# Optimization experiments

Measured on AMD Instinct MI355X. Metric: run time of the kernel, lower is better.

## Reference

```python
import jax, jax.numpy as jnp
import numpy as np

DIM = 256
H = 4
K = 16
R = 4
EPS = 1e-5


def _conv1x1(x, W, b):
    # x: [B, Cin, N, P], W: [Cout, Cin], b: [Cout]
    return jnp.einsum('oc,bcnp->bonp', W, x) + b[None, :, None, None]


def setup_inputs() -> dict:
    key = jax.random.key(0)
    ks = jax.random.split(key, 12)
    B, N = 4, 8192
    s = 1.0 / np.sqrt(DIM)
    inp = {
        'queries': jax.random.normal(ks[0], (B, DIM, N, R), dtype=jnp.float32),
        'feats': jax.random.normal(ks[1], (B, DIM, N, K), dtype=jnp.float32),
        'Wq': jax.random.normal(ks[2], (DIM, DIM), dtype=jnp.float32) * s,
        'bq': jnp.zeros((DIM,), dtype=jnp.float32),
        'Wk': jax.random.normal(ks[3], (DIM, DIM), dtype=jnp.float32) * s,
        'bk': jnp.zeros((DIM,), dtype=jnp.float32),
        'Wv': jax.random.normal(ks[4], (DIM, DIM), dtype=jnp.float32) * s,
        'bv': jnp.zeros((DIM,), dtype=jnp.float32),
        'W1': jax.random.normal(ks[5], (2 * DIM, DIM), dtype=jnp.float32) * s,
        'b1': jnp.zeros((2 * DIM,), dtype=jnp.float32),
        'gamma': jnp.ones((2 * DIM,), dtype=jnp.float32),
        'beta': jnp.zeros((2 * DIM,), dtype=jnp.float32),
        'W2': jax.random.normal(ks[6], (DIM, 2 * DIM), dtype=jnp.float32) * (1.0 / np.sqrt(2 * DIM)),
        'b2': jnp.zeros((DIM,), dtype=jnp.float32),
    }
    return inp


def reference(queries, feats, Wq, bq, Wk, bk, Wv, bv, W1, b1, gamma, beta, W2, b2):
    B, _, N, _ = feats.shape
    d = DIM // H
    queries_iden = queries  # [B, dim, N, r]

    q = _conv1x1(queries, Wq, bq).reshape(B, H, d, N, R)   # [B,h,d,N,r]
    k = _conv1x1(feats, Wk, bk).reshape(B, H, d, N, K)     # [B,h,d,N,K]
    v = _conv1x1(feats, Wv, bv).reshape(B, H, d, N, K)     # [B,h,d,N,K]

    # logits: [B,N,h,r,K]
    logits = jnp.einsum('bhdnr,bhdnk->bnhrk', q, k) * (d ** -0.5)
    soft = jax.nn.softmax(logits, axis=-1)
    # agg: [B,N,h,r,d] -> permute to [B,N,h,d,r] -> [B,N,dim,r] -> [B,dim,N,r]
    agg = jnp.einsum('bnhrk,bhdnk->bnhdr', soft, v)
    agg = agg.reshape(B, N, DIM, R).transpose(0, 2, 1, 3)
    agg = agg + queries_iden

    # FFN: conv1x1 -> BN (training-mode batch stats) -> ReLU -> conv1x1, residual, ReLU
    h1 = _conv1x1(agg, W1, b1)  # [B, 2*dim, N, r]
    mean = jnp.mean(h1, axis=(0, 2, 3), keepdims=True)
    var = jnp.var(h1, axis=(0, 2, 3), keepdims=True)
    h1 = (h1 - mean) * jax.lax.rsqrt(var + EPS)
    h1 = h1 * gamma[None, :, None, None] + beta[None, :, None, None]
    h1 = jax.nn.relu(h1)
    h2 = _conv1x1(h1, W2, b2)
    return jax.nn.relu(h2 + agg)
```

## Files before the change

kernel.cpp:

```cpp
#include <hip/hip_runtime.h>
#include <hip/hip_bf16.h>

#define NB 4
#define NRQ 32768
#define NKF 131072

using u16 = unsigned short;
typedef short bf16x8 __attribute__((ext_vector_type(8)));
typedef float f32x4  __attribute__((ext_vector_type(4)));
typedef u16   u16x8  __attribute__((ext_vector_type(8)));
typedef u16   u16x4  __attribute__((ext_vector_type(4)));
typedef u16   u16x2  __attribute__((ext_vector_type(2)));

#if defined(__has_builtin)
#  if __has_builtin(__builtin_amdgcn_fdot2_f32_bf16)
#    define HAVE_DOT2 1
#  endif
#endif
#ifndef HAVE_DOT2
#  define HAVE_DOT2 0
#endif

#if HAVE_DOT2
typedef __bf16 bfv2 __attribute__((ext_vector_type(2)));
union bpack { bf16x8 v; bfv2 p[4]; };
__device__ __forceinline__ float dot2(bfv2 a, bfv2 b, float c){
  return __builtin_amdgcn_fdot2_f32_bf16(a, b, c, false);
}
#endif
union vpack { bf16x8 v; u16 e[8]; };

__device__ __forceinline__ u16 f2b(float f){
  unsigned u = __float_as_uint(f);
  return (u16)((u + 0x7fffu + ((u >> 16) & 1u)) >> 16);
}
__device__ __forceinline__ float b2f(u16 v){
  return __uint_as_float(((unsigned)v) << 16);
}

#define GLOAD16(g, l) __builtin_amdgcn_global_load_lds( \
    (const __attribute__((address_space(1))) unsigned int*)(g), \
    (__attribute__((address_space(3))) unsigned int*)(l), 16, 0, 0)

__global__ __launch_bounds__(256) void cvtW_k(
    const float* __restrict__ Wk, const float* __restrict__ Wv,
    const float* __restrict__ Wq, const float* __restrict__ W1,
    const float* __restrict__ W2, u16* __restrict__ wT)
{
  long e = ((long)blockIdx.x * 256 + threadIdx.x) * 8;
  const float* src; long off;
  if      (e < 65536)  { src = Wk; off = e; }
  else if (e < 131072) { src = Wv; off = e - 65536; }
  else if (e < 196608) { src = Wq; off = e - 131072; }
  else if (e < 327680) { src = W1; off = e - 196608; }
  else                 { src = W2; off = e - 327680; }
  float4 f0 = *reinterpret_cast<const float4*>(src + off);
  float4 f1 = *reinterpret_cast<const float4*>(src + off + 4);
  u16x8 p;
  p[0]=f2b(f0.x); p[1]=f2b(f0.y); p[2]=f2b(f0.z); p[3]=f2b(f0.w);
  p[4]=f2b(f1.x); p[5]=f2b(f1.y); p[6]=f2b(f1.z); p[7]=f2b(f1.w);
  *reinterpret_cast<u16x8*>(wT + e) = p;
}

__global__ void prep_k(const float* __restrict__ bk, const float* __restrict__ bv,
                       float* __restrict__ bKV, float* __restrict__ stats)
{
  int i = blockIdx.x * 256 + threadIdx.x;
  if (i < 512)       bKV[i] = (i < 256) ? bk[i] : bv[i - 256];
  else               stats[i - 512] = 0.f;
}

__global__ __launch_bounds__(256) void transpose_k(
    const float* __restrict__ in, u16* __restrict__ out,
    int NCtot, long outBatch)
{
  __shared__ u16 sT[64][264];
  const int t = threadIdx.x, b = blockIdx.y;
  const int nr0 = blockIdx.x * 64;
  const int cb = t >> 2, nrq = t & 3;
  const long ib = (long)b * 256 * NCtot + nr0;

  #pragma unroll
  for (int ci = 0; ci < 4; ++ci){
    const int c = cb + ci * 64;
    const float* src = in + ib + (long)c * NCtot + nrq * 16;
    #pragma unroll
    for (int j = 0; j < 4; ++j){
      float4 f = *reinterpret_cast<const float4*>(src + j * 4);
      int nr = nrq * 16 + j * 4;
      sT[nr+0][c] = f2b(f.x); sT[nr+1][c] = f2b(f.y);
      sT[nr+2][c] = f2b(f.z); sT[nr+3][c] = f2b(f.w);
    }
  }
  __syncthreads();
  const int row = t >> 2, qtr = t & 3;
  u16* orow = out + (long)b * outBatch + (long)(nr0 + row) * 256 + qtr * 64;
  #pragma unroll
  for (int i = 0; i < 8; ++i)
    *reinterpret_cast<u16x8*>(orow + i * 8) =
        *reinterpret_cast<const u16x8*>(&sT[row][qtr * 64 + i * 8]);
}

template<int MODE, int KD>
__global__ __launch_bounds__(256) void gemm_k(
    const u16* __restrict__ A, long aBatch, int chTiles,
    const u16* __restrict__ Wb, const float* __restrict__ bias,
    u16* __restrict__ outH, long oBatch, int NCH,
    float* __restrict__ statSum, float* __restrict__ statSq,
    const u16* __restrict__ residT,
    float* __restrict__ outF, long fBatch)
{
  __shared__ __align__(16) char sA[2][16384];
  __shared__ __align__(16) char sB[2][16384];

  const int t = threadIdx.x, lane = t & 63, wid = t >> 6;
  const int wm = wid >> 1, wn = wid & 1;
  const int b = blockIdx.z;

  const int nwg = gridDim.x, orig = blockIdx.x;
  const int qq = nwg >> 3, rr = nwg & 7, xcd = orig & 7, pos = orig >> 3;
  const int wg = (xcd < rr ? xcd * (qq + 1) : rr * (qq + 1) + (xcd - rr) * qq) + pos;
  const int rowT = wg / chTiles, chT = wg % chTiles;

  const u16* Ab = A + (long)b * aBatch + (long)rowT * 128 * KD;
  const u16* Wt = Wb + (long)chT * 128 * KD;
  const int sub = lane >> 3, kc8 = ((lane & 7) ^ sub) * 8;

  f32x4 acc[4][4];
  #pragma unroll
  for (int i = 0; i < 4; ++i)
    #pragma unroll
    for (int j = 0; j < 4; ++j) acc[i][j] = (f32x4){0.f,0.f,0.f,0.f};

  auto STAGE = [&](int buf, int ks){
    const int k0 = ks * 64;
    #pragma unroll
    for (int i = 0; i < 4; ++i){
      const int chunk = wid * 4 + i;
      GLOAD16(Ab + (long)(chunk*8 + sub)*KD + k0 + kc8, sA[buf] + chunk*1024);
      GLOAD16(Wt + (long)(chunk*8 + sub)*KD + k0 + kc8, sB[buf] + chunk*1024);
    }
  };

  constexpr int NT = KD / 64;
  STAGE(0, 0);
  __syncthreads();
  int cur = 0;
  for (int ks = 0; ks < NT; ++ks){
    if (ks + 1 < NT) STAGE(cur ^ 1, ks + 1);
    const char* pA = sA[cur]; const char* pB = sB[cur];
    #pragma unroll
    for (int kk = 0; kk < 2; ++kk){
      bf16x8 af[4], bf[4];
      #pragma unroll
      for (int mi = 0; mi < 4; ++mi){
        int m = wm*64 + mi*16 + (lane & 15);
        af[mi] = *reinterpret_cast<const bf16x8*>(
            pA + ((m*128 + kk*64 + (lane>>4)*16) ^ ((m & 7) << 4)));
      }
      #pragma unroll
      for (int ni = 0; ni < 4; ++ni){
        int c = wn*64 + ni*16 + (lane & 15);
        bf[ni] = *reinterpret_cast<const bf16x8*>(
            pB + ((c*128 + kk*64 + (lane>>4)*16) ^ ((c & 7) << 4)));
      }
      #pragma unroll
      for (int mi = 0; mi < 4; ++mi)
        #pragma unroll
        for (int ni = 0; ni < 4; ++ni)
          acc[mi][ni] = __builtin_amdgcn_mfma_f32_16x16x32_bf16(
              af[mi], bf[ni], acc[mi][ni], 0, 0, 0);
    }
    __syncthreads();
    cur ^= 1;
  }

  int chI[4]; float bv[4];
  #pragma unroll
  for (int ni = 0; ni < 4; ++ni){
    int ch = chT*128 + wn*64 + ni*16 + (lane & 15);
    chI[ni] = ch;
    bv[ni] = bias[ch];
  }
  if (MODE <= 1){
    float s[4] = {0,0,0,0}, sq[4] = {0,0,0,0};
    u16* outb = outH + (long)b * oBatch;
    #pragma unroll
    for (int mi = 0; mi < 4; ++mi){
      #pragma unroll
      for (int j = 0; j < 4; ++j){
        const long row = rowT*128 + wm*64 + mi*16 + (lane>>4)*4 + j;
        #pragma unroll
        for (int ni = 0; ni < 4; ++ni){
          float v = acc[mi][ni][j] + bv[ni];
          outb[row * NCH + chI[ni]] = f2b(v);
          if (MODE == 1){ s[ni] += v; sq[ni] += v * v; }
        }
      }
    }
    if (MODE == 1){
      #pragma unroll
      for (int ni = 0; ni < 4; ++ni){
        s[ni]  += __shfl_xor(s[ni], 16);  s[ni]  += __shfl_xor(s[ni], 32);
        sq[ni] += __shfl_xor(sq[ni], 16); sq[ni] += __shfl_xor(sq[ni], 32);
      }
      if (lane < 16){
        #pragma unroll
        for (int ni = 0; ni < 4; ++ni){
          atomicAdd(&statSum[chI[ni]], s[ni]);
          atomicAdd(&statSq[chI[ni]],  sq[ni]);
        }
      }
    }
  } else {
    const u16* rb = residT + (long)b * ((long)NRQ * 256);
    #pragma unroll
    for (int mi = 0; mi < 4; ++mi){
      const int nr0 = rowT*128 + wm*64 + mi*16 + (lane>>4)*4;
      #pragma unroll
      for (int ni = 0; ni < 4; ++ni){
        float4 o;
        o.x = fmaxf(acc[mi][ni][0] + bv[ni] + b2f(rb[(long)(nr0+0)*256 + chI[ni]]), 0.f);
        o.y = fmaxf(acc[mi][ni][1] + bv[ni] + b2f(rb[(long)(nr0+1)*256 + chI[ni]]), 0.f);
        o.z = fmaxf(acc[mi][ni][2] + bv[ni] + b2f(rb[(long)(nr0+2)*256 + chI[ni]]), 0.f);
        o.w = fmaxf(acc[mi][ni][3] + bv[ni] + b2f(rb[(long)(nr0+3)*256 + chI[ni]]), 0.f);
        *reinterpret_cast<float4*>(outF + (long)b*fBatch + (long)chI[ni]*NRQ + nr0) = o;
      }
    }
  }
}

__global__ __launch_bounds__(512, 4) void kvattn_k(
    const float* __restrict__ feats, const u16* __restrict__ wKV,
    const float* __restrict__ bKV, const u16* __restrict__ qT,
    const u16* __restrict__ qrT, u16* __restrict__ aggT)
{
  __shared__ __align__(16) char LDS[73728];
  char* sAg = LDS;
  char* sW  = LDS + 8192;
  char* sK  = LDS;
  char* sVT = LDS + 33792;
#if HAVE_DOT2
  char* sSb = LDS + 66560;
#else
  float* sS = (float*)(LDS + 66560);
#endif

  const int t = threadIdx.x, lane = t & 63, wid = t >> 6;
  const int wr = wid >> 2, wc = wid & 3;
  const int b = blockIdx.y;
  const long row0 = (long)blockIdx.x * 64;

  const int chL = t >> 4, nq = t & 15;
  const float* fbase = feats + (long)b * 256 * NKF + row0 + nq * 4;

  auto STAGEW = [&](int buf, int ks){
    const int k0 = ks * 32;
    #pragma unroll
    for (int i = 0; i < 4; ++i){
      const int cw = wid * 4 + i;
      const int ch = cw * 16 + (lane >> 2), jd = lane & 3;
      GLOAD16(wKV + (long)ch * 256 + k0 + ((jd ^ ((ch >> 1) & 3)) * 8),
              sW + buf * 32768 + cw * 1024);
    }
  };
  auto WRITEA = [&](int buf, float4 f){
    #pragma unroll
    for (int i = 0; i < 4; ++i){
      const int r = nq * 4 + i;
      const int byte = buf*4096 + r*64 + ((((chL>>3) ^ ((r>>1)&3))) << 4) + (chL & 7)*2;
      float e = (i == 0) ? f.x : (i == 1) ? f.y : (i == 2) ? f.z : f.w;
      *reinterpret_cast<u16*>(sAg + byte) = f2b(e);
    }
  };

  f32x4 acc[2][8];
  #pragma unroll
  for (int i = 0; i < 2; ++i)
    #pragma unroll
    for (int j = 0; j < 8; ++j) acc[i][j] = (f32x4){0.f,0.f,0.f,0.f};

  {
    float4 a0 = *reinterpret_cast<const float4*>(fbase + (long)chL * NKF);
    STAGEW(0, 0);
    WRITEA(0, a0);
  }
  __syncthreads();
  int cur = 0;
  for (int ks = 0; ks < 8; ++ks){
    float4 an;
    if (ks < 7){
      an = *reinterpret_cast<const float4*>(fbase + (long)((ks+1)*32 + chL) * NKF);
      STAGEW(cur ^ 1, ks + 1);
    }
    const char* pA = sAg + cur * 4096;
    const char* pW = sW  + cur * 32768;
    bf16x8 af[2];
    #pragma unroll
    for (int mi = 0; mi < 2; ++mi){
      const int m = wr*32 + mi*16 + (lane & 15);
      af[mi] = *reinterpret_cast<const bf16x8*>(
          pA + m*64 + (((lane>>4) ^ ((m>>1)&3)) * 16));
    }
    #pragma unroll
    for (int ni = 0; ni < 8; ++ni){
      const int ch = wc*128 + ni*16 + (lane & 15);
      bf16x8 bf = *reinterpret_cast<const bf16x8*>(
          pW + ch*64 + (((lane>>4) ^ ((ch>>1)&3)) * 16));
      acc[0][ni] = __builtin_amdgcn_mfma_f32_16x16x32_bf16(af[0], bf, acc[0][ni], 0,0,0);
      acc[1][ni] = __builtin_amdgcn_mfma_f32_16x16x32_bf16(af[1], bf, acc[1][ni], 0,0,0);
    }
    if (ks < 7) WRITEA(cur ^ 1, an);
    __syncthreads();
    cur ^= 1;
  }

  {
    float bv[8];
    #pragma unroll
    for (int ni = 0; ni < 8; ++ni) bv[ni] = bKV[wc*128 + ni*16 + (lane & 15)];
    if (wc < 2){
      #pragma unroll
      for (int mi = 0; mi < 2; ++mi){
        const int p2 = wr*2 + mi;
        #pragma unroll
        for (int ni = 0; ni < 8; ++ni){
          const int ch = wc*128 + ni*16 + (lane & 15);
          #pragma unroll
          for (int j = 0; j < 4; ++j){
            const int kk2 = (lane>>4)*4 + j;
            *reinterpret_cast<u16*>(sK + (p2*16 + kk2)*528 + ch*2) =
                f2b(acc[mi][ni][j] + bv[ni]);
          }
        }
      }
    } else {
      #pragma unroll
      for (int mi = 0; mi < 2; ++mi){
        const int p2 = wr*2 + mi;
        #pragma unroll
        for (int ni = 0; ni < 8; ++ni){
          const int cv = (wc-2)*128 + ni*16 + (lane & 15);
          u16x4 w;
          #pragma unroll
          for (int j = 0; j < 4; ++j) w[j] = f2b(acc[mi][ni][j] + bv[ni]);
          *reinterpret_cast<u16x4*>(sVT + p2*8192 + cv*32 + (lane>>4)*8) = w;
        }
      }
    }
  }
  __syncthreads();

  const int p = wid & 3, rh = wid >> 2;
  const int nqg = blockIdx.x * 4 + p;
  {
    const int h = lane >> 4, kk = lane & 15;
    const u16* qb = qT + ((long)b*NRQ + (long)nqg*4 + rh*2)*256 + h*64;
    const char* kr = sK + (p*16 + kk)*528 + h*128;
    float l0 = 0.f, l1 = 0.f;
#if HAVE_DOT2
    #pragma unroll
    for (int d8 = 0; d8 < 8; ++d8){
      bpack K8, Q0, Q1;
      K8.v = *reinterpret_cast<const bf16x8*>(kr + d8*16);
      Q0.v = *reinterpret_cast<const bf16x8*>(qb + d8*8);
      Q1.v = *reinterpret_cast<const bf16x8*>(qb + 256 + d8*8);
      #pragma unroll
      for (int pi = 0; pi < 4; ++pi){
        l0 = dot2(K8.p[pi], Q0.p[pi], l0);
        l1 = dot2(K8.p[pi], Q1.p[pi], l1);
      }
    }
#else
    #pragma unroll
    for (int d8 = 0; d8 < 8; ++d8){
      vpack K8, Q0, Q1;
      K8.v = *reinterpret_cast<const bf16x8*>(kr + d8*16);
      Q0.v = *reinterpret_cast<const bf16x8*>(qb + d8*8);
      Q1.v = *reinterpret_cast<const bf16x8*>(qb + 256 + d8*8);
      #pragma unroll
      for (int e = 0; e < 8; ++e){
        float kf = b2f(K8.e[e]);
        l0 = fmaf(kf, b2f(Q0.e[e]), l0);
        l1 = fmaf(kf, b2f(Q1.e[e]), l1);
      }
    }
#endif
    float pr[2]; float lv[2] = {l0, l1};
    #pragma unroll
    for (int r = 0; r < 2; ++r){
      float x = lv[r] * 0.125f;
      float m = x;
      #pragma unroll
      for (int off = 1; off < 16; off <<= 1) m = fmaxf(m, __shfl_xor(m, off));
      float e = __expf(x - m);
      float ssum = e;
      #pragma unroll
      for (int off = 1; off < 16; off <<= 1) ssum += __shfl_xor(ssum, off);
      pr[r] = e / ssum;
    }
#if HAVE_DOT2
    float o0 = __shfl_xor(pr[0], 1), o1 = __shfl_xor(pr[1], 1);
    if (!(kk & 1)){
      char* sb = sSb + (p*4 + h)*128 + (kk>>1)*4;
      u16x2 w0; w0[0] = f2b(pr[0]); w0[1] = f2b(o0);
      u16x2 w1; w1[0] = f2b(pr[1]); w1[1] = f2b(o1);
      *reinterpret_cast<u16x2*>(sb + (rh*2)*32)     = w0;
      *reinterpret_cast<u16x2*>(sb + (rh*2 + 1)*32) = w1;
    }
#else
    *reinterpret_cast<float2*>(sS + ((p*4 + h)*16 + kk)*4 + rh*2) =
        make_float2(pr[0], pr[1]);
#endif
  }
  __syncthreads();

  {
    const int cv0 = rh*128 + lane*2;
    const int h = cv0 >> 6;
    const char* vb = sVT + p*8192 + cv0*32;
    float ar[4][2];
#if HAVE_DOT2
    bpack va0, va1, vc0, vc1;
    va0.v = *reinterpret_cast<const bf16x8*>(vb);
    va1.v = *reinterpret_cast<const bf16x8*>(vb + 16);
    vc0.v = *reinterpret_cast<const bf16x8*>(vb + 32);
    vc1.v = *reinterpret_cast<const bf16x8*>(vb + 48);
    #pragma unroll
    for (int r = 0; r < 4; ++r){
      bpack s0, s1;
      const char* sb = sSb + (p*4 + h)*128 + r*32;
      s0.v = *reinterpret_cast<const bf16x8*>(sb);
      s1.v = *reinterpret_cast<const bf16x8*>(sb + 16);
      float a0 = 0.f, a1 = 0.f;
      #pragma unroll
      for (int pi = 0; pi < 4; ++pi){
        a0 = dot2(va0.p[pi], s0.p[pi], a0);
        a1 = dot2(vc0.p[pi], s0.p[pi], a1);
      }
      #pragma unroll
      for (int pi = 0; pi < 4; ++pi){
        a0 = dot2(va1.p[pi], s1.p[pi], a0);
        a1 = dot2(vc1.p[pi], s1.p[pi], a1);
      }
      ar[r][0] = a0; ar[r][1] = a1;
    }
#else
    vpack va0, va1, vc0, vc1;
    va0.v = *reinterpret_cast<const bf16x8*>(vb);
    va1.v = *reinterpret_cast<const bf16x8*>(vb + 16);
    vc0.v = *reinterpret_cast<const bf16x8*>(vb + 32);
    vc1.v = *reinterpret_cast<const bf16x8*>(vb + 48);
    #pragma unroll
    for (int r = 0; r < 4; ++r){ ar[r][0] = 0.f; ar[r][1] = 0.f; }
    #pragma unroll
    for (int kk = 0; kk < 16; ++kk){
      float v0 = b2f(kk < 8 ? va0.e[kk & 7] : va1.e[kk & 7]);
      float v1 = b2f(kk < 8 ? vc0.e[kk & 7] : vc1.e[kk & 7]);
      float4 sv = *reinterpret_cast<const float4*>(sS + ((p*4 + h)*16 + kk)*4);
      ar[0][0] += sv.x*v0; ar[0][1] += sv.x*v1;
      ar[1][0] += sv.y*v0; ar[1][1] += sv.y*v1;
      ar[2][0] += sv.z*v0; ar[2][1] += sv.z*v1;
      ar[3][0] += sv.w*v0; ar[3][1] += sv.w*v1;
    }
#endif
    const u16* rq = qrT + ((long)b*NRQ + (long)nqg*4)*256 + cv0;
    u16* ob = aggT + ((long)b*NRQ + (long)nqg*4)*256 + cv0;
    #pragma unroll
    for (int r = 0; r < 4; ++r){
      u16x2 q2 = *reinterpret_cast<const u16x2*>(rq + r*256);
      u16x2 pk;
      pk[0] = f2b(ar[r][0] + b2f(q2[0]));
      pk[1] = f2b(ar[r][1] + b2f(q2[1]));
      *reinterpret_cast<u16x2*>(ob + r*256) = pk;
    }
  }
}

__global__ void bnrelu_k(u16* __restrict__ h1, const float* __restrict__ sc,
                         const float* __restrict__ sh)
{
  const long total = (long)NB * NRQ * 512 / 8;
  for (long i = (long)blockIdx.x * blockDim.x + threadIdx.x; i < total;
       i += (long)gridDim.x * blockDim.x){
    u16x8 v = *reinterpret_cast<const u16x8*>(h1 + i * 8);
    int chb = (int)((i * 8) & 511);
    float4 s0 = *reinterpret_cast<const float4*>(sc + chb);
    float4 s1 = *reinterpret_cast<const float4*>(sc + chb + 4);
    float4 h0 = *reinterpret_cast<const float4*>(sh + chb);
    float4 h1v= *reinterpret_cast<const float4*>(sh + chb + 4);
    u16x8 o;
    o[0]=f2b(fmaxf(b2f(v[0])*s0.x+h0.x ,0.f)); o[1]=f2b(fmaxf(b2f(v[1])*s0.y+h0.y ,0.f));
    o[2]=f2b(fmaxf(b2f(v[2])*s0.z+h0.z ,0.f)); o[3]=f2b(fmaxf(b2f(v[3])*s0.w+h0.w ,0.f));
    o[4]=f2b(fmaxf(b2f(v[4])*s1.x+h1v.x,0.f)); o[5]=f2b(fmaxf(b2f(v[5])*s1.y+h1v.y,0.f));
    o[6]=f2b(fmaxf(b2f(v[6])*s1.z+h1v.z,0.f)); o[7]=f2b(fmaxf(b2f(v[7])*s1.w+h1v.w,0.f));
    *reinterpret_cast<u16x8*>(h1 + i * 8) = o;
  }
}

__global__ void finalize_k(const float* __restrict__ st,
                           const float* __restrict__ gamma,
                           const float* __restrict__ beta,
                           float* __restrict__ out)
{
  int o = blockIdx.x*256 + threadIdx.x;
  const float inv = 1.f / 131072.f;
  float mean = st[o] * inv;
  float var  = st[512 + o] * inv - mean*mean;
  float sc   = gamma[o] * rsqrtf(var + 1e-5f);
  out[o]       = sc;
  out[512 + o] = beta[o] - mean * sc;
}

extern "C" void kernel_launch(void* const* d_in, const int* in_sizes, int n_in,
                              void* d_out, int out_size, void* d_ws, size_t ws_size,
                              hipStream_t stream)
{
  (void)in_sizes; (void)n_in; (void)out_size; (void)ws_size;
  const float* queries = (const float*)d_in[0];
  const float* feats   = (const float*)d_in[1];
  const float* Wq = (const float*)d_in[2];
  const float* bq = (const float*)d_in[3];
  const float* Wk = (const float*)d_in[4];
  const float* bk = (const float*)d_in[5];
  const float* Wv = (const float*)d_in[6];
  const float* bv = (const float*)d_in[7];
  const float* W1 = (const float*)d_in[8];
  const float* b1 = (const float*)d_in[9];
  const float* gamma = (const float*)d_in[10];
  const float* beta  = (const float*)d_in[11];
  const float* W2 = (const float*)d_in[12];
  const float* b2 = (const float*)d_in[13];

  char* ws = (char*)d_ws;
  u16*   h1T   = (u16*)ws;
  u16*   qrT   = (u16*)(ws + 134217728L);
  u16*   qT    = (u16*)(ws + 201326592L);
  u16*   aggT  = (u16*)(ws + 268435456L);
  float* stats = (float*)(ws + 335544320L);
  float* scale = stats + 1024;
  float* shift = stats + 1536;
  u16*   wT    = (u16*)(ws + 335552512L);
  u16*   wKV   = wT;
  u16*   wQ    = wT + 131072;
  u16*   wW1   = wT + 196608;
  u16*   wW2   = wT + 327680;
  float* bKV   = (float*)(wT + 458752);

  cvtW_k<<<dim3(224), 256, 0, stream>>>(Wk, Wv, Wq, W1, W2, wT);
  prep_k<<<dim3(6), 256, 0, stream>>>(bk, bv, bKV, stats);

  transpose_k<<<dim3(NRQ/64, NB), 256, 0, stream>>>(queries, qrT, NRQ, (long)NRQ*256);

  gemm_k<0, 256><<<dim3(512, 1, NB), 256, 0, stream>>>(
      qrT, (long)NRQ*256, 2, wQ, bq,
      qT, (long)NRQ*256, 256, nullptr, nullptr, nullptr, nullptr, 0);

  kvattn_k<<<dim3(NKF/64, NB), 512, 0, stream>>>(feats, wKV, bKV, qT, qrT, aggT);

  gemm_k<1, 256><<<dim3(1024, 1, NB), 256, 0, stream>>>(
      aggT, (long)NRQ*256, 4, wW1, b1,
      h1T, (long)NRQ*512, 512, stats, stats + 512, nullptr, nullptr, 0);

  finalize_k<<<dim3(2), 256, 0, stream>>>(stats, gamma, beta, scale);

  bnrelu_k<<<dim3(2048), 256, 0, stream>>>(h1T, scale, shift);

  gemm_k<2, 512><<<dim3(512, 1, NB), 256, 0, stream>>>(
      h1T, (long)NRQ*512, 2, wW2, b2,
      nullptr, 0, 256, nullptr, nullptr, aggT, (float*)d_out, (long)256*NRQ);
}
```

Baseline: 683.9 us.

## Fuse BN+ReLU into W2 GEMM A-load and rework kvattn LDS layouts

Result: faster. 649.3 us (-5.1%).

```diff
diff --git a/kernel.cpp b/kernel.cpp
--- a/kernel.cpp
+++ b/kernel.cpp
@@ -107,6 +107,7 @@
     const u16* __restrict__ Wb, const float* __restrict__ bias,
     u16* __restrict__ outH, long oBatch, int NCH,
     float* __restrict__ statSum, float* __restrict__ statSq,
+    const float* __restrict__ xsc, const float* __restrict__ xsh,
     const u16* __restrict__ residT,
     float* __restrict__ outF, long fBatch)
 {
@@ -134,11 +135,41 @@
 
   auto STAGE = [&](int buf, int ks){
     const int k0 = ks * 64;
-    #pragma unroll
-    for (int i = 0; i < 4; ++i){
-      const int chunk = wid * 4 + i;
-      GLOAD16(Ab + (long)(chunk*8 + sub)*KD + k0 + kc8, sA[buf] + chunk*1024);
-      GLOAD16(Wt + (long)(chunk*8 + sub)*KD + k0 + kc8, sB[buf] + chunk*1024);
+    if constexpr (MODE == 3){
+      const int wrow = t >> 1, whalf = t & 1;
+      const u16* arow = Ab + (long)wrow * KD + k0 + whalf * 32;
+      #pragma unroll
+      for (int i = 0; i < 4; ++i){
+        u16x8 v = *reinterpret_cast<const u16x8*>(arow + i * 8);
+        const int kb = k0 + whalf*32 + i*8;
+        float4 s0 = *reinterpret_cast<const float4*>(xsc + kb);
+        float4 s1 = *reinterpret_cast<const float4*>(xsc + kb + 4);
+        float4 h0 = *reinterpret_cast<const float4*>(xsh + kb);
+        float4 h1 = *reinterpret_cast<const float4*>(xsh + kb + 4);
+        u16x8 o;
+        o[0]=f2b(fmaxf(b2f(v[0])*s0.x+h0.x,0.f));
+        o[1]=f2b(fmaxf(b2f(v[1])*s0.y+h0.y,0.f));
+        o[2]=f2b(fmaxf(b2f(v[2])*s0.z+h0.z,0.f));
+        o[3]=f2b(fmaxf(b2f(v[3])*s0.w+h0.w,0.f));
+        o[4]=f2b(fmaxf(b2f(v[4])*s1.x+h1.x,0.f));
+        o[5]=f2b(fmaxf(b2f(v[5])*s1.y+h1.y,0.f));
+        o[6]=f2b(fmaxf(b2f(v[6])*s1.z+h1.z,0.f));
+        o[7]=f2b(fmaxf(b2f(v[7])*s1.w+h1.w,0.f));
+        *reinterpret_cast<u16x8*>(
+            sA[buf] + ((wrow*128 + whalf*64 + i*16) ^ ((wrow & 7) << 4))) = o;
+      }
+      #pragma unroll
+      for (int i = 0; i < 4; ++i){
+        const int chunk = wid * 4 + i;
+        GLOAD16(Wt + (long)(chunk*8 + sub)*KD + k0 + kc8, sB[buf] + chunk*1024);
+      }
+    } else {
+      #pragma unroll
+      for (int i = 0; i < 4; ++i){
+        const int chunk = wid * 4 + i;
+        GLOAD16(Ab + (long)(chunk*8 + sub)*KD + k0 + kc8, sA[buf] + chunk*1024);
+        GLOAD16(Wt + (long)(chunk*8 + sub)*KD + k0 + kc8, sB[buf] + chunk*1024);
+      }
     }
   };
 
@@ -236,15 +267,11 @@
     const u16* __restrict__ qrT, u16* __restrict__ aggT)
 {
   __shared__ __align__(16) char LDS[73728];
-  char* sAg = LDS;
-  char* sW  = LDS + 8192;
-  char* sK  = LDS;
-  char* sVT = LDS + 33792;
-#if HAVE_DOT2
-  char* sSb = LDS + 66560;
-#else
-  float* sS = (float*)(LDS + 66560);
-#endif
+  char*  sAg = LDS;
+  char*  sW  = LDS + 8192;
+  char*  sK  = LDS;
+  char*  sV  = LDS + 33792;
+  float* sSf = (float*)(LDS + 67072);
 
   const int t = threadIdx.x, lane = t & 63, wid = t >> 6;
   const int wr = wid >> 2, wc = wid & 3;
@@ -268,7 +295,8 @@
     #pragma unroll
     for (int i = 0; i < 4; ++i){
       const int r = nq * 4 + i;
-      const int byte = buf*4096 + r*64 + ((((chL>>3) ^ ((r>>1)&3))) << 4) + (chL & 7)*2;
+      const int byte = buf*4096 + r*64
+                     + (((chL>>3) ^ ((r>>2)&3)) << 4) + (chL & 7)*2;
       float e = (i == 0) ? f.x : (i == 1) ? f.y : (i == 2) ? f.z : f.w;
       *reinterpret_cast<u16*>(sAg + byte) = f2b(e);
     }
@@ -300,7 +328,7 @@
     for (int mi = 0; mi < 2; ++mi){
       const int m = wr*32 + mi*16 + (lane & 15);
       af[mi] = *reinterpret_cast<const bf16x8*>(
-          pA + m*64 + (((lane>>4) ^ ((m>>1)&3)) * 16));
+          pA + m*64 + (((lane>>4) ^ ((m>>2)&3)) * 16));
     }
     #pragma unroll
     for (int ni = 0; ni < 8; ++ni){
@@ -329,7 +357,8 @@
           #pragma unroll
           for (int j = 0; j < 4; ++j){
             const int kk2 = (lane>>4)*4 + j;
-            *reinterpret_cast<u16*>(sK + (p2*16 + kk2)*528 + ch*2) =
+            *reinterpret_cast<u16*>(
+                sK + (p2*16 + kk2)*528 + ((ch*2) ^ ((kk2 & 7) << 4))) =
                 f2b(acc[mi][ni][j] + bv[ni]);
           }
         }
@@ -341,10 +370,12 @@
         #pragma unroll
         for (int ni = 0; ni < 8; ++ni){
           const int cv = (wc-2)*128 + ni*16 + (lane & 15);
-          u16x4 w;
           #pragma unroll
-          for (int j = 0; j < 4; ++j) w[j] = f2b(acc[mi][ni][j] + bv[ni]);
-          *reinterpret_cast<u16x4*>(sVT + p2*8192 + cv*32 + (lane>>4)*8) = w;
+          for (int j = 0; j < 4; ++j){
+            const int kk2 = (lane>>4)*4 + j;
+            *reinterpret_cast<u16*>(sV + (p2*16 + kk2)*520 + cv*2) =
+                f2b(acc[mi][ni][j] + bv[ni]);
+          }
         }
       }
     }
@@ -356,13 +387,14 @@
   {
     const int h = lane >> 4, kk = lane & 15;
     const u16* qb = qT + ((long)b*NRQ + (long)nqg*4 + rh*2)*256 + h*64;
-    const char* kr = sK + (p*16 + kk)*528 + h*128;
+    const char* kr = sK + (p*16 + kk)*528;
     float l0 = 0.f, l1 = 0.f;
 #if HAVE_DOT2
     #pragma unroll
     for (int d8 = 0; d8 < 8; ++d8){
       bpack K8, Q0, Q1;
-      K8.v = *reinterpret_cast<const bf16x8*>(kr + d8*16);
+      K8.v = *reinterpret_cast<const bf16x8*>(
+          kr + ((h*128 + d8*16) ^ ((kk & 7) << 4)));
       Q0.v = *reinterpret_cast<const bf16x8*>(qb + d8*8);
       Q1.v = *reinterpret_cast<const bf16x8*>(qb + 256 + d8*8);
       #pragma unroll
@@ -375,7 +407,8 @@
     #pragma unroll
     for (int d8 = 0; d8 < 8; ++d8){
       vpack K8, Q0, Q1;
-      K8.v = *reinterpret_cast<const bf16x8*>(kr + d8*16);
+      K8.v = *reinterpret_cast<const bf16x8*>(
+          kr + ((h*128 + d8*16) ^ ((kk & 7) << 4)));
       Q0.v = *reinterpret_cast<const bf16x8*>(qb + d8*8);
       Q1.v = *reinterpret_cast<const bf16x8*>(qb + 256 + d8*8);
       #pragma unroll
@@ -399,102 +432,37 @@
       for (int off = 1; off < 16; off <<= 1) ssum += __shfl_xor(ssum, off);
       pr[r] = e / ssum;
     }
-#if HAVE_DOT2
-    float o0 = __shfl_xor(pr[0], 1), o1 = __shfl_xor(pr[1], 1);
-    if (!(kk & 1)){
-      char* sb = sSb + (p*4 + h)*128 + (kk>>1)*4;
-      u16x2 w0; w0[0] = f2b(pr[0]); w0[1] = f2b(o0);
-      u16x2 w1; w1[0] = f2b(pr[1]); w1[1] = f2b(o1);
-      *reinterpret_cast<u16x2*>(sb + (rh*2)*32)     = w0;
-      *reinterpret_cast<u16x2*>(sb + (rh*2 + 1)*32) = w1;
-    }
-#else
-    *reinterpret_cast<float2*>(sS + ((p*4 + h)*16 + kk)*4 + rh*2) =
+    *reinterpret_cast<float2*>(sSf + (p*4 + h)*68 + kk*4 + rh*2) =
         make_float2(pr[0], pr[1]);
-#endif
   }
   __syncthreads();
 
   {
-    const int cv0 = rh*128 + lane*2;
-    const int h = cv0 >> 6;
-    const char* vb = sVT + p*8192 + cv0*32;
-    float ar[4][2];
-#if HAVE_DOT2
-    bpack va0, va1, vc0, vc1;
-    va0.v = *reinterpret_cast<const bf16x8*>(vb);
-    va1.v = *reinterpret_cast<const bf16x8*>(vb + 16);
-    vc0.v = *reinterpret_cast<const bf16x8*>(vb + 32);
-    vc1.v = *reinterpret_cast<const bf16x8*>(vb + 48);
-    #pragma unroll
-    for (int r = 0; r < 4; ++r){
-      bpack s0, s1;
-      const char* sb = sSb + (p*4 + h)*128 + r*32;
-      s0.v = *reinterpret_cast<const bf16x8*>(sb);
-      s1.v = *reinterpret_cast<const bf16x8*>(sb + 16);
-      float a0 = 0.f, a1 = 0.f;
-      #pragma unroll
-      for (int pi = 0; pi < 4; ++pi){
-        a0 = dot2(va0.p[pi], s0.p[pi], a0);
-        a1 = dot2(vc0.p[pi], s0.p[pi], a1);
-      }
-      #pragma unroll
-      for (int pi = 0; pi < 4; ++pi){
-        a0 = dot2(va1.p[pi], s1.p[pi], a0);
-        a1 = dot2(vc1.p[pi], s1.p[pi], a1);
-      }
-      ar[r][0] = a0; ar[r][1] = a1;
-    }
-#else
-    vpack va0, va1, vc0, vc1;
-    va0.v = *reinterpret_cast<const bf16x8*>(vb);
-    va1.v = *reinterpret_cast<const bf16x8*>(vb + 16);
-    vc0.v = *reinterpret_cast<const bf16x8*>(vb + 32);
-    vc1.v = *reinterpret_cast<const bf16x8*>(vb + 48);
-    #pragma unroll
-    for (int r = 0; r < 4; ++r){ ar[r][0] = 0.f; ar[r][1] = 0.f; }
+    const int c0 = rh*128 + lane*2;
+    const int h = c0 >> 6;
+    const char* vrow = sV + (p*16)*520;
+    const float* ss = sSf + (p*4 + h)*68;
+    float a[4][2] = {};
     #pragma unroll
     for (int kk = 0; kk < 16; ++kk){
-      float v0 = b2f(kk < 8 ? va0.e[kk & 7] : va1.e[kk & 7]);
-      float v1 = b2f(kk < 8 ? vc0.e[kk & 7] : vc1.e[kk & 7]);
-      float4 sv = *reinterpret_cast<const float4*>(sS + ((p*4 + h)*16 + kk)*4);
-      ar[0][0] += sv.x*v0; ar[0][1] += sv.x*v1;
-      ar[1][0] += sv.y*v0; ar[1][1] += sv.y*v1;
-      ar[2][0] += sv.z*v0; ar[2][1] += sv.z*v1;
-      ar[3][0] += sv.w*v0; ar[3][1] += sv.w*v1;
-    }
-#endif
-    const u16* rq = qrT + ((long)b*NRQ + (long)nqg*4)*256 + cv0;
-    u16* ob = aggT + ((long)b*NRQ + (long)nqg*4)*256 + cv0;
+      u16x2 vv = *reinterpret_cast<const u16x2*>(vrow + kk*520 + c0*2);
+      float4 sv = *reinterpret_cast<const float4*>(ss + kk*4);
+      float v0 = b2f(vv[0]), v1 = b2f(vv[1]);
+      a[0][0] += sv.x*v0; a[0][1] += sv.x*v1;
+      a[1][0] += sv.y*v0; a[1][1] += sv.y*v1;
+      a[2][0] += sv.z*v0; a[2][1] += sv.z*v1;
+      a[3][0] += sv.w*v0; a[3][1] += sv.w*v1;
+    }
+    const u16* rq = qrT + ((long)b*NRQ + (long)nqg*4)*256 + c0;
+    u16* ob = aggT + ((long)b*NRQ + (long)nqg*4)*256 + c0;
     #pragma unroll
     for (int r = 0; r < 4; ++r){
       u16x2 q2 = *reinterpret_cast<const u16x2*>(rq + r*256);
       u16x2 pk;
-      pk[0] = f2b(ar[r][0] + b2f(q2[0]));
-      pk[1] = f2b(ar[r][1] + b2f(q2[1]));
+      pk[0] = f2b(a[r][0] + b2f(q2[0]));
+      pk[1] = f2b(a[r][1] + b2f(q2[1]));
       *reinterpret_cast<u16x2*>(ob + r*256) = pk;
     }
-  }
-}
-
-__global__ void bnrelu_k(u16* __restrict__ h1, const float* __restrict__ sc,
-                         const float* __restrict__ sh)
-{
-  const long total = (long)NB * NRQ * 512 / 8;
-  for (long i = (long)blockIdx.x * blockDim.x + threadIdx.x; i < total;
-       i += (long)gridDim.x * blockDim.x){
-    u16x8 v = *reinterpret_cast<const u16x8*>(h1 + i * 8);
-    int chb = (int)((i * 8) & 511);
-    float4 s0 = *reinterpret_cast<const float4*>(sc + chb);
-    float4 s1 = *reinterpret_cast<const float4*>(sc + chb + 4);
-    float4 h0 = *reinterpret_cast<const float4*>(sh + chb);
-    float4 h1v= *reinterpret_cast<const float4*>(sh + chb + 4);
-    u16x8 o;
-    o[0]=f2b(fmaxf(b2f(v[0])*s0.x+h0.x ,0.f)); o[1]=f2b(fmaxf(b2f(v[1])*s0.y+h0.y ,0.f));
-    o[2]=f2b(fmaxf(b2f(v[2])*s0.z+h0.z ,0.f)); o[3]=f2b(fmaxf(b2f(v[3])*s0.w+h0.w ,0.f));
-    o[4]=f2b(fmaxf(b2f(v[4])*s1.x+h1v.x,0.f)); o[5]=f2b(fmaxf(b2f(v[5])*s1.y+h1v.y,0.f));
-    o[6]=f2b(fmaxf(b2f(v[6])*s1.z+h1v.z,0.f)); o[7]=f2b(fmaxf(b2f(v[7])*s1.w+h1v.w,0.f));
-    *reinterpret_cast<u16x8*>(h1 + i * 8) = o;
   }
 }
 
@@ -554,19 +522,20 @@
 
   gemm_k<0, 256><<<dim3(512, 1, NB), 256, 0, stream>>>(
       qrT, (long)NRQ*256, 2, wQ, bq,
-      qT, (long)NRQ*256, 256, nullptr, nullptr, nullptr, nullptr, 0);
+      qT, (long)NRQ*256, 256, nullptr, nullptr, nullptr, nullptr,
+      nullptr, nullptr, 0);
 
   kvattn_k<<<dim3(NKF/64, NB), 512, 0, stream>>>(feats, wKV, bKV, qT, qrT, aggT);
 
   gemm_k<1, 256><<<dim3(1024, 1, NB), 256, 0, stream>>>(
       aggT, (long)NRQ*256, 4, wW1, b1,
-      h1T, (long)NRQ*512, 512, stats, stats + 512, nullptr, nullptr, 0);
+      h1T, (long)NRQ*512, 512, stats, stats + 512, nullptr, nullptr,
+      nullptr, nullptr, 0);
 
   finalize_k<<<dim3(2), 256, 0, stream>>>(stats, gamma, beta, scale);
 
-  bnrelu_k<<<dim3(2048), 256, 0, stream>>>(h1T, scale, shift);
-
-  gemm_k<2, 512><<<dim3(512, 1, NB), 256, 0, stream>>>(
+  gemm_k<3, 512><<<dim3(512, 1, NB), 256, 0, stream>>>(
       h1T, (long)NRQ*512, 2, wW2, b2,
-      nullptr, 0, 256, nullptr, nullptr, aggT, (float*)d_out, (long)256*NRQ);
-}
+      nullptr, 0, 256, nullptr, nullptr, scale, shift,
+      aggT, (float*)d_out, (long)256*NRQ);
+}
```
